# Performance work log

Hardware: AMD Instinct MI355X
Metric: run time of the kernel (lower is better)

The kernel has to match this reference:

```python
import jax, jax.numpy as jnp
import numpy as np

CROP_H = 14
CROP_W = 14
EXTRAP = 0.0  # extrapolation_value


def setup_inputs() -> dict:
    key = jax.random.key(0)
    k1, k2, k3 = jax.random.split(key, 3)
    image = jax.random.normal(k1, (8, 256, 200, 304), dtype=jnp.float32)
    boxes = jax.random.uniform(k2, (1000, 4), dtype=jnp.float32)  # normalized [y1,x1,y2,x2]
    box_indices = jax.random.randint(k3, (1000,), 0, 8, dtype=jnp.int32)
    return {"image": image, "boxes": boxes, "box_indices": box_indices}


def _sample_coords(lo, hi, size, crop_size, dtype):
    # TF crop_and_resize coordinate mapping (normalized box -> pixel coords)
    if crop_size > 1:
        step = (hi - lo) * (size - 1) / (crop_size - 1)            # [N]
        return lo[:, None] * (size - 1) + jnp.arange(crop_size, dtype=dtype) * step[:, None]  # [N, crop]
    else:
        return 0.5 * (lo + hi)[:, None] * (size - 1)


def _crop_and_resize(image, boxes, box_indices):
    B, C, H, W = image.shape
    dt = image.dtype
    y1, x1, y2, x2 = boxes[:, 0], boxes[:, 1], boxes[:, 2], boxes[:, 3]

    in_y = _sample_coords(y1, y2, H, CROP_H, dt)   # [N, CROP_H]
    in_x = _sample_coords(x1, x2, W, CROP_W, dt)   # [N, CROP_W]

    valid_y = (in_y >= 0) & (in_y <= H - 1)        # [N, CROP_H]
    valid_x = (in_x >= 0) & (in_x <= W - 1)        # [N, CROP_W]

    top_f = jnp.floor(in_y)
    left_f = jnp.floor(in_x)
    y_lerp = in_y - top_f                          # [N, CROP_H]
    x_lerp = in_x - left_f                         # [N, CROP_W]

    top = jnp.clip(top_f, 0, H - 1).astype(jnp.int32)
    bot = jnp.clip(jnp.ceil(in_y), 0, H - 1).astype(jnp.int32)
    left = jnp.clip(left_f, 0, W - 1).astype(jnp.int32)
    right = jnp.clip(jnp.ceil(in_x), 0, W - 1).astype(jnp.int32)

    b = box_indices[:, None, None]                 # [N,1,1]

    def gather(yi, xi):
        # advanced indexing: result [N, CROP_H, CROP_W, C]
        return image[b, :, yi[:, :, None], xi[:, None, :]]

    tl = gather(top, left)
    tr = gather(top, right)
    bl = gather(bot, left)
    br = gather(bot, right)

    xl = x_lerp[:, None, :, None]                  # [N,1,CROP_W,1]
    yl = y_lerp[:, :, None, None]                  # [N,CROP_H,1,1]
    top_v = tl + (tr - tl) * xl
    bot_v = bl + (br - bl) * xl
    out = top_v + (bot_v - top_v) * yl             # [N,CROP_H,CROP_W,C]

    valid = valid_y[:, :, None, None] & valid_x[:, None, :, None]
    out = jnp.where(valid, out, jnp.asarray(EXTRAP, dt))
    return jnp.transpose(out, (0, 3, 1, 2))        # [N, C, CROP_H, CROP_W]


def reference(image, boxes, box_indices):
    return _crop_and_resize(image, boxes, box_indices)
```

## Files before the change

### kernel.cpp

```cpp
#include <hip/hip_runtime.h>

#define CROP  14
#define POS   196
#define HH    200
#define WW    304
#define CC    256
#define NIMG  8
#define TR    25
#define NT    8
#define NBIN  (NIMG*NT)
#define TSZ   (26*WW)


__device__ __forceinline__ int top_row(float y1, float y2, int yy) {
    const float in_y = y1*199.0f + (float)yy*((y2-y1)*199.0f*(1.0f/13.0f));
    return (int)fminf(fmaxf(floorf(in_y), 0.0f), 199.0f);
}

__global__ __launch_bounds__(1024) void prep(
    const float* __restrict__ boxes, const int* __restrict__ bidx, int n_boxes,
    unsigned* __restrict__ counts, unsigned* __restrict__ offsets,
    unsigned* __restrict__ cursors)
{
    __shared__ unsigned scnt[NBIN];
    const int t = threadIdx.x;
    if (t < NBIN) scnt[t] = 0;
    __syncthreads();
    for (int n = t; n < n_boxes; n += 1024) {
        const float y1 = boxes[4*n+0], y2 = boxes[4*n+2];
        const int b = bidx[n];
        int prev = -1, yyLo = 0;
        for (int yy = 0; yy < 14; ++yy) {
            const int tile = top_row(y1, y2, yy) / TR;
            if (tile != prev) {
                if (prev >= 0) atomicAdd(&scnt[b*NT+prev], (unsigned)((yy-yyLo)*CROP));
                prev = tile; yyLo = yy;
            }
        }
        atomicAdd(&scnt[b*NT+prev], (unsigned)((14-yyLo)*CROP));
    }
    __syncthreads();
    if (t == 0) {
        unsigned acc = 0;
        for (int i = 0; i < NBIN; ++i) {
            const unsigned c = scnt[i];
            counts[i] = c; offsets[i] = acc; cursors[i] = acc; acc += c;
        }
    }
}

__global__ __launch_bounds__(256) void emit_desc(
    const float* __restrict__ boxes, const int* __restrict__ bidx,
    unsigned* __restrict__ cursors, int4* __restrict__ desc)
{
    __shared__ int rowSlot[14];
    const int n = blockIdx.x;
    const int t = threadIdx.x;
    const float y1 = boxes[4*n+0], x1 = boxes[4*n+1];
    const float y2 = boxes[4*n+2], x2 = boxes[4*n+3];
    const int b = bidx[n];

    if (t == 0) {
        int tiles[14];
        for (int yy = 0; yy < 14; ++yy) tiles[yy] = top_row(y1, y2, yy) / TR;
        for (int yy = 0; yy < 14; ++yy) {
            if (yy == 0 || tiles[yy] != tiles[yy-1]) {
                int hi = yy;
                while (hi+1 < 14 && tiles[hi+1] == tiles[yy]) ++hi;
                const unsigned base = atomicAdd(&cursors[b*NT + tiles[yy]],
                                                (unsigned)((hi-yy+1)*CROP));
                for (int r = yy; r <= hi; ++r) rowSlot[r] = (int)base + (r-yy)*CROP;
            }
        }
    }
    __syncthreads();

    if (t < POS) {
        const int yy = t / CROP, xx = t - yy*CROP;
        const float in_y = y1*199.0f + (float)yy*((y2-y1)*199.0f*(1.0f/13.0f));
        const float in_x = x1*303.0f + (float)xx*((x2-x1)*303.0f*(1.0f/13.0f));
        const float tf = floorf(in_y), lf = floorf(in_x);
        const int topc   = (int)fminf(fmaxf(tf,          0.0f), 199.0f);
        const int botc   = (int)fminf(fmaxf(ceilf(in_y), 0.0f), 199.0f);
        const int leftc  = (int)fminf(fmaxf(lf,          0.0f), 303.0f);
        const int rightc = (int)fminf(fmaxf(ceilf(in_x), 0.0f), 303.0f);
        const int tile = topc / TR;
        const int r0   = topc - tile*TR;
        const unsigned w0 = (unsigned)(r0*WW + leftc)
                          | ((unsigned)(rightc - leftc) << 13)
                          | ((unsigned)(botc - topc)    << 14)
                          | ((unsigned)((in_y >= 0.0f) & (in_y <= 199.0f) &
                                        (in_x >= 0.0f) & (in_x <= 303.0f)) << 15);
        int4 d;
        d.x = (int)w0;
        d.y = n*CC*POS + t;
        d.z = __float_as_int(in_x - lf);
        d.w = __float_as_int(in_y - tf);
        desc[rowSlot[yy] + xx] = d;
    }
}

__global__ __launch_bounds__(512) void crop_compute(
    const float*    __restrict__ image,
    const unsigned* __restrict__ counts,
    const unsigned* __restrict__ offsets,
    const int4*     __restrict__ desc,
    float*          __restrict__ out)
{
    __shared__ float tile[2 * TSZ];
    const int c0  = blockIdx.x * 2;
    const int bin = blockIdx.y;
    const int b   = bin >> 3;
    const int tl  = bin & 7;
    const int t   = threadIdx.x;
    const int base = tl * TR;
    const int rows = (tl == NT-1) ? TR : TR + 1;

    const int S    = (int)counts[bin];
    const int off0 = (int)offsets[bin];

    {
        const float* src = image + ((size_t)b*CC + (size_t)c0)*(size_t)(HH*WW)
                                 + (size_t)base*WW;
        const int nv = (rows * WW) >> 2;
        const float4* s4a = (const float4*)src;
        const float4* s4b = (const float4*)(src + HH*WW);
        float4* t4a = (float4*)tile;
        float4* t4b = (float4*)(tile + TSZ);
        for (int i = t; i < nv; i += 512) { t4a[i] = s4a[i]; t4b[i] = s4b[i]; }
    }
    __syncthreads();
    if (S == 0) return;

    const size_t cb0 = (size_t)c0 * POS;
    for (int k = t; k < S; k += 512) {
        const int4 d = desc[off0 + k];
        const unsigned w0 = (unsigned)d.x;
        const int off = (int)(w0 & 0x1FFFu);
        const int dx  = (int)((w0 >> 13) & 1u);
        const int dyw = ((w0 >> 14) & 1u) ? WW : 0;
        const float xl = __int_as_float(d.z);
        const float yl = __int_as_float(d.w);

        const float* p0 = tile + off;
        const float* p1 = p0 + TSZ;
        const float tl0 = p0[0];
        const float tr0 = p0[dx];
        const float bl0 = p0[dyw];
        const float br0 = p0[dyw + dx];
        const float tl1 = p1[0];
        const float tr1 = p1[dx];
        const float bl1 = p1[dyw];
        const float br1 = p1[dyw + dx];

        const float tv0 = tl0 + (tr0 - tl0) * xl;
        const float bv0 = bl0 + (br0 - bl0) * xl;
        const float tv1 = tl1 + (tr1 - tl1) * xl;
        const float bv1 = bl1 + (br1 - bl1) * xl;
        float v0 = tv0 + (bv0 - tv0) * yl;
        float v1 = tv1 + (bv1 - tv1) * yl;
        if (!(w0 & 0x8000u)) { v0 = 0.0f; v1 = 0.0f; }

        const size_t o = (size_t)(unsigned)d.y + cb0;
        out[o]       = v0;
        out[o + POS] = v1;
    }
}

extern "C" void kernel_launch(void* const* d_in, const int* in_sizes, int n_in,
                              void* d_out, int out_size, void* d_ws, size_t ws_size,
                              hipStream_t stream) {
    const float* image = (const float*)d_in[0];
    const float* boxes = (const float*)d_in[1];
    const int*   bidx  = (const int*)d_in[2];
    float*       out   = (float*)d_out;
    const int n_boxes = in_sizes[1] / 4;

    unsigned* counts  = (unsigned*)d_ws;
    unsigned* offsets = counts + 64;
    unsigned* cursors = counts + 128;
    int4*     desc    = (int4*)((char*)d_ws + 1024);

    prep<<<dim3(1), dim3(1024), 0, stream>>>(boxes, bidx, n_boxes, counts, offsets, cursors);
    emit_desc<<<dim3(n_boxes), dim3(256), 0, stream>>>(boxes, bidx, cursors, desc);
    crop_compute<<<dim3(CC/2, NBIN), dim3(512), 0, stream>>>(image, counts, offsets, desc, out);
}
```

Measured before the change: 199.7 us.

## Use smaller row tiles with four channels per block in crop kernel

Row tiles shrink from 25 to 13 rows, giving 16 tiles per image, and each block now loads and interpolates four channels instead of two. Every descriptor read is therefore reused across four channels, which halves descriptor traffic and the number of blocks along the channel axis. Smaller tiles keep the shared-memory footprint about the same and balance work more finely. The cost is more halo-row reloading and more rows split across tiles, plus higher register use per thread.

```diff
diff --git a/kernel.cpp b/kernel.cpp
--- a/kernel.cpp
+++ b/kernel.cpp
@@ -6,10 +6,10 @@
 #define WW    304
 #define CC    256
 #define NIMG  8
-#define TR    25
-#define NT    8
+#define TR    13
+#define NT    16
 #define NBIN  (NIMG*NT)
-#define TSZ   (26*WW)
+#define TSZ   (14*WW)
 
 
 __device__ __forceinline__ int top_row(float y1, float y2, int yy) {
@@ -107,14 +107,14 @@
     const int4*     __restrict__ desc,
     float*          __restrict__ out)
 {
-    __shared__ float tile[2 * TSZ];
-    const int c0  = blockIdx.x * 2;
+    __shared__ float tile[4 * TSZ];
+    const int c0  = blockIdx.x * 4;
     const int bin = blockIdx.y;
-    const int b   = bin >> 3;
-    const int tl  = bin & 7;
+    const int b   = bin >> 4;
+    const int tl  = bin & 15;
     const int t   = threadIdx.x;
     const int base = tl * TR;
-    const int rows = (tl == NT-1) ? TR : TR + 1;
+    const int rows = (tl == NT-1) ? (HH - (NT-1)*TR) : (TR + 1);
 
     const int S    = (int)counts[bin];
     const int off0 = (int)offsets[bin];
@@ -124,10 +124,16 @@
                                  + (size_t)base*WW;
         const int nv = (rows * WW) >> 2;
         const float4* s4a = (const float4*)src;
-        const float4* s4b = (const float4*)(src + HH*WW);
+        const float4* s4b = (const float4*)(src +     HH*WW);
+        const float4* s4c = (const float4*)(src + 2 * HH*WW);
+        const float4* s4d = (const float4*)(src + 3 * HH*WW);
         float4* t4a = (float4*)tile;
-        float4* t4b = (float4*)(tile + TSZ);
-        for (int i = t; i < nv; i += 512) { t4a[i] = s4a[i]; t4b[i] = s4b[i]; }
+        float4* t4b = (float4*)(tile +     TSZ);
+        float4* t4c = (float4*)(tile + 2 * TSZ);
+        float4* t4d = (float4*)(tile + 3 * TSZ);
+        for (int i = t; i < nv; i += 512) {
+            t4a[i] = s4a[i]; t4b[i] = s4b[i]; t4c[i] = s4c[i]; t4d[i] = s4d[i];
+        }
     }
     __syncthreads();
     if (S == 0) return;
@@ -144,26 +150,34 @@
 
         const float* p0 = tile + off;
         const float* p1 = p0 + TSZ;
-        const float tl0 = p0[0];
-        const float tr0 = p0[dx];
-        const float bl0 = p0[dyw];
-        const float br0 = p0[dyw + dx];
-        const float tl1 = p1[0];
-        const float tr1 = p1[dx];
-        const float bl1 = p1[dyw];
-        const float br1 = p1[dyw + dx];
+        const float* p2 = p0 + 2*TSZ;
+        const float* p3 = p0 + 3*TSZ;
+
+        const float tl0 = p0[0],  tr0 = p0[dx], bl0 = p0[dyw], br0 = p0[dyw+dx];
+        const float tl1 = p1[0],  tr1 = p1[dx], bl1 = p1[dyw], br1 = p1[dyw+dx];
+        const float tl2 = p2[0],  tr2 = p2[dx], bl2 = p2[dyw], br2 = p2[dyw+dx];
+        const float tl3 = p3[0],  tr3 = p3[dx], bl3 = p3[dyw], br3 = p3[dyw+dx];
 
         const float tv0 = tl0 + (tr0 - tl0) * xl;
         const float bv0 = bl0 + (br0 - bl0) * xl;
         const float tv1 = tl1 + (tr1 - tl1) * xl;
         const float bv1 = bl1 + (br1 - bl1) * xl;
+        const float tv2 = tl2 + (tr2 - tl2) * xl;
+        const float bv2 = bl2 + (br2 - bl2) * xl;
+        const float tv3 = tl3 + (tr3 - tl3) * xl;
+        const float bv3 = bl3 + (br3 - bl3) * xl;
+
         float v0 = tv0 + (bv0 - tv0) * yl;
         float v1 = tv1 + (bv1 - tv1) * yl;
-        if (!(w0 & 0x8000u)) { v0 = 0.0f; v1 = 0.0f; }
+        float v2 = tv2 + (bv2 - tv2) * yl;
+        float v3 = tv3 + (bv3 - tv3) * yl;
+        if (!(w0 & 0x8000u)) { v0 = 0.0f; v1 = 0.0f; v2 = 0.0f; v3 = 0.0f; }
 
         const size_t o = (size_t)(unsigned)d.y + cb0;
-        out[o]       = v0;
-        out[o + POS] = v1;
+        out[o]         = v0;
+        out[o +   POS] = v1;
+        out[o + 2*POS] = v2;
+        out[o + 3*POS] = v3;
     }
 }
 
@@ -177,11 +191,11 @@
     const int n_boxes = in_sizes[1] / 4;
 
     unsigned* counts  = (unsigned*)d_ws;
-    unsigned* offsets = counts + 64;
-    unsigned* cursors = counts + 128;
-    int4*     desc    = (int4*)((char*)d_ws + 1024);
+    unsigned* offsets = counts + 128;
+    unsigned* cursors = counts + 256;
+    int4*     desc    = (int4*)((char*)d_ws + 2048);
 
     prep<<<dim3(1), dim3(1024), 0, stream>>>(boxes, bidx, n_boxes, counts, offsets, cursors);
     emit_desc<<<dim3(n_boxes), dim3(256), 0, stream>>>(boxes, bidx, cursors, desc);
-    crop_compute<<<dim3(CC/2, NBIN), dim3(512), 0, stream>>>(image, counts, offsets, desc, out);
-}
+    crop_compute<<<dim3(CC/4, NBIN), dim3(512), 0, stream>>>(image, counts, offsets, desc, out);
+}
```

New measurement: 187.4 us. 1.07x faster.
